# Performance work log

Hardware: AMD Instinct MI355X
Metric: run time of the kernel (lower is better)

Reference implementation:

```python
import jax, jax.numpy as jnp
import numpy as np

N, C, D, H = 4096, 64, 128, 4
CD = 2 * D          # combined_dim = 2*input_size
DQ = CD // 8        # per-head query/key dim


def _mlp(x, W1, b1, W2, b2):
    # MLP(in, hidden, out): Linear -> ReLU -> Linear
    return jax.nn.relu(x @ W1.T + b1) @ W2.T + b2


def _gru(x, h, Wih, bih, Whh, bhh):
    # torch.nn.GRUCell math
    gi = x @ Wih.T + bih
    gh = h @ Whh.T + bhh
    ir, iz, inn = jnp.split(gi, 3, axis=-1)
    hr, hz, hn = jnp.split(gh, 3, axis=-1)
    r = jax.nn.sigmoid(ir + hr)
    z = jax.nn.sigmoid(iz + hz)
    n = jnp.tanh(inn + r * hn)
    return (1.0 - z) * n + z * h


def setup_inputs() -> dict:
    key = jax.random.key(0)
    ks = jax.random.split(key, 16)
    def w(k, shape, fan):
        return jax.random.normal(k, shape, jnp.float32) / np.float32(np.sqrt(fan))
    return {
        "x": jax.random.normal(ks[0], (N, D), jnp.float32),
        "h": jax.random.normal(ks[1], (N, D), jnp.float32),
        "cluster_h": jax.random.normal(ks[2], (C, D), jnp.float32),
        "query_vectors": jax.random.normal(ks[3], (C, D), jnp.float32),
        "cluster_labels": jax.random.randint(ks[4], (N,), 0, C),
        "nodes_ind": jnp.arange(N),
        "edge_index_intra": jax.random.randint(ks[5], (2, 1024), 0, N),
        "num_clusters": C,
        "Wq": w(ks[6], (H, DQ, CD), CD), "bq": jnp.zeros((H, DQ), jnp.float32),
        "Wk": w(ks[7], (H, DQ, CD), CD), "bk": jnp.zeros((H, DQ), jnp.float32),
        "Wv": w(ks[8], (H, CD, CD), CD), "bv": jnp.zeros((H, CD), jnp.float32),
        "W1": w(ks[9], (CD, H * CD), H * CD), "b1": jnp.zeros((CD,), jnp.float32),
        "W2": w(ks[10], (CD, CD), CD), "b2": jnp.zeros((CD,), jnp.float32),
        "gru_Wih": w(ks[11], (3 * D, D), D), "gru_bih": jnp.zeros((3 * D,), jnp.float32),
        "gru_Whh": w(ks[12], (3 * D, D), D), "gru_bhh": jnp.zeros((3 * D,), jnp.float32),
        "Wp": 0.1 * w(ks[13], (D, D), D), "bp": jnp.zeros((D,), jnp.float32),
    }


def reference(x, h, cluster_h, query_vectors, cluster_labels, nodes_ind,
              edge_index_intra, num_clusters,
              Wq, bq, Wk, bk, Wv, bv, W1, b1, W2, b2,
              gru_Wih, gru_bih, gru_Whh, gru_bhh, Wp, bp):
    combined = jnp.concatenate([x, h], axis=-1)              # [N, 2D]
    # multi-head dense attention over all nodes (heads vectorized)
    q = jnp.einsum('nd,hed->hne', combined, Wq) + bq[:, None, :]   # [H,N,DQ]
    k = jnp.einsum('nd,hed->hne', combined, Wk) + bk[:, None, :]
    v = jnp.einsum('nd,hed->hne', combined, Wv) + bv[:, None, :]   # [H,N,2D]
    scores = jnp.einsum('hne,hme->hnm', q, k) / jnp.sqrt(jnp.float32(DQ))
    attn = jax.nn.softmax(jax.nn.leaky_relu(scores, 0.2), axis=-1)  # [H,N,N]
    hp = jnp.einsum('hnm,hme->hne', attn, v)                 # [H,N,2D]
    hp = jnp.transpose(hp, (1, 0, 2)).reshape(combined.shape[0], -1)  # [N,H*2D]
    node_repr = _mlp(hp, W1, b1, W2, b2) + combined          # [N,2D]
    # per-cluster mean of previous node hidden states
    ones = jnp.ones((h.shape[0],), h.dtype)
    counts = jax.ops.segment_sum(ones, cluster_labels, num_segments=num_clusters)
    sums = jax.ops.segment_sum(h, cluster_labels, num_segments=num_clusters)
    agg = sums / jnp.maximum(counts, 1.0)[:, None]           # [C,D]
    present = (counts > 0)[:, None]
    new_ch = _gru(agg, cluster_h, gru_Wih, gru_bih, gru_Whh, gru_bhh)
    updated_cluster_h = jnp.where(present, new_ch, cluster_h)  # [C,D]
    # cluster-to-node projection broadcast back to nodes
    c2n = (updated_cluster_h @ Wp.T + bp)[cluster_labels]    # [N,D]
    updated_h = node_repr[:, D:] + c2n                       # [N,D]
    return updated_h, updated_cluster_h
```

## Files before the change

kernel.cpp:

```cpp
#include <hip/hip_runtime.h>
#include <math.h>

#define N_NODES 4096
#define NHEADS  4
#define NSPLIT  4
#define KVRANGE 1024

typedef _Float16 f16;
typedef _Float16 half8 __attribute__((ext_vector_type(8)));
typedef float f32x4 __attribute__((ext_vector_type(4)));

__global__ __launch_bounds__(256) void k_combined(const float* __restrict__ x,
                                                  const float* __restrict__ h,
                                                  f16* __restrict__ comb16) {
  int i = blockIdx.x * blockDim.x + threadIdx.x;
  int n = i >> 6, c = i & 63;
  float4 v;
  if (c < 32) v = ((const float4*)x)[n * 32 + c];
  else        v = ((const float4*)h)[n * 32 + (c - 32)];
  union { uint2 u; f16 h4[4]; } pk;
  pk.h4[0] = (f16)v.x; pk.h4[1] = (f16)v.y; pk.h4[2] = (f16)v.z; pk.h4[3] = (f16)v.w;
  *(uint2*)&comb16[(size_t)i * 4] = pk.u;
}

__global__ __launch_bounds__(256) void k_w2h(const float* __restrict__ Wq,
                                             const float* __restrict__ Wk,
                                             const float* __restrict__ Wv,
                                             const float* __restrict__ W1,
                                             const float* __restrict__ W2,
                                             f16* __restrict__ pool) {
  int i4 = (blockIdx.x * 256 + threadIdx.x) * 4;
  const float* src; int off;
  if      (i4 <  32768) { src = Wq; off = 0; }
  else if (i4 <  65536) { src = Wk; off = 32768; }
  else if (i4 < 327680) { src = Wv; off = 65536; }
  else if (i4 < 589824) { src = W1; off = 327680; }
  else                  { src = W2; off = 589824; }
  float4 v = *(const float4*)&src[i4 - off];
  union { uint2 u; f16 h4[4]; } pk;
  pk.h4[0] = (f16)v.x; pk.h4[1] = (f16)v.y; pk.h4[2] = (f16)v.z; pk.h4[3] = (f16)v.w;
  *(uint2*)&pool[i4] = pk.u;
}

template <int EPI>
__global__ __launch_bounds__(256) void k_gemm16(const f16* __restrict__ A,
                                                const f16* __restrict__ B,
                                                const float* __restrict__ bias,
                                                const float* __restrict__ resid,
                                                void* __restrict__ outv,
                                                int M, int K, int J, float alpha) {
  __shared__ f16 As[64 * 64];
  __shared__ f16 Bs[64 * 64];
  const int t  = threadIdx.x;
  const int mb = blockIdx.x * 64, jb = blockIdx.y * 64;
  const int w  = t >> 6, l = t & 63;
  const int g_ = l >> 4, c_ = l & 15;
  const int m0 = (w >> 1) * 32, n0 = (w & 1) * 32;

  f32x4 acc[2][2];
#pragma unroll
  for (int i = 0; i < 2; ++i)
#pragma unroll
    for (int j = 0; j < 2; ++j) acc[i][j] = (f32x4){0.f, 0.f, 0.f, 0.f};

#define FRAG16(BUF, row, kh) \
  (*(const half8*)&BUF[(size_t)(row) * 64 + (((((kh) * 4 + g_) ^ (c_ & 7))) << 3)])

  for (int kb = 0; kb < K; kb += 64) {
    __syncthreads();
#pragma unroll
    for (int i = 0; i < 2; ++i) {
      int f = t + i * 256;
      int r = f >> 3, ch = f & 7;
      *(uint4*)&As[r * 64 + ((ch ^ (r & 7)) << 3)] =
          *(const uint4*)&A[(size_t)(mb + r) * K + kb + ch * 8];
      *(uint4*)&Bs[r * 64 + ((ch ^ (r & 7)) << 3)] =
          *(const uint4*)&B[(size_t)(jb + r) * K + kb + ch * 8];
    }
    __syncthreads();
#pragma unroll
    for (int kh = 0; kh < 2; ++kh) {
      half8 a0 = FRAG16(As, m0 + c_, kh);
      half8 a1 = FRAG16(As, m0 + 16 + c_, kh);
      half8 b0 = FRAG16(Bs, n0 + c_, kh);
      half8 b1 = FRAG16(Bs, n0 + 16 + c_, kh);
      acc[0][0] = __builtin_amdgcn_mfma_f32_16x16x32_f16(a0, b0, acc[0][0], 0, 0, 0);
      acc[0][1] = __builtin_amdgcn_mfma_f32_16x16x32_f16(a0, b1, acc[0][1], 0, 0, 0);
      acc[1][0] = __builtin_amdgcn_mfma_f32_16x16x32_f16(a1, b0, acc[1][0], 0, 0, 0);
      acc[1][1] = __builtin_amdgcn_mfma_f32_16x16x32_f16(a1, b1, acc[1][1], 0, 0, 0);
    }
  }
#undef FRAG16

#pragma unroll
  for (int mt = 0; mt < 2; ++mt)
#pragma unroll
    for (int nt = 0; nt < 2; ++nt) {
      int mbase = mb + m0 + mt * 16 + g_ * 4;
      int jj    = jb + n0 + nt * 16 + c_;
      if (EPI == 0 || EPI == 1) {
        f16* out = (f16*)outv;
        float bc = bias[jj];
#pragma unroll
        for (int r = 0; r < 4; ++r) {
          float v = (acc[mt][nt][r] + bc) * alpha;
          if (EPI == 1) v = fmaxf(v, 0.f);
          out[(size_t)(mbase + r) * J + jj] = (f16)v;
        }
      } else if (EPI == 2) {
        f16* out = (f16*)outv;
#pragma unroll
        for (int r = 0; r < 4; ++r)
          out[(size_t)(mbase + r) * J + jj] = (f16)(acc[mt][nt][r] + bias[mbase + r]);
      } else {
        float* out = (float*)outv;
        float bc = bias[jj];
#pragma unroll
        for (int r = 0; r < 4; ++r)
          out[(size_t)(mbase + r) * J + jj] =
              acc[mt][nt][r] + bc + resid[(size_t)(mbase + r) * J + jj];
      }
    }
}

__global__ __launch_bounds__(256, 4) void k_attn_mfma(const f16* __restrict__ qg,
                                                      const f16* __restrict__ kg,
                                                      const f16* __restrict__ vt,
                                                      f16* __restrict__ pO,
                                                      float* __restrict__ pM,
                                                      float* __restrict__ pL) {
  const int hd  = blockIdx.y;
  const int sp  = blockIdx.z;
  const int kv0 = sp * KVRANGE;
  const int t   = threadIdx.x;
  const int w   = t >> 6, l = t & 63;
  const int g   = l >> 4, c = l & 15;
  const int qb  = blockIdx.x * 64 + w * 16;

  __shared__ f16 Ks[32 * 40];
  __shared__ f16 Vs[256 * 40];

  half8 qf = *(const half8*)&qg[(size_t)(qb + c) * 128 + hd * 32 + g * 8];

  f32x4 oacc[16];
#pragma unroll
  for (int i = 0; i < 16; ++i) oacc[i] = (f32x4){0.f, 0.f, 0.f, 0.f};
  float m_run = -INFINITY, l_run = 0.f;

  const int  srcA  = (((2 * g) & 3) << 4) + c;
  const int  srcB  = (((2 * g + 1) & 3) << 4) + c;
  const bool selhi = (g >> 1) != 0;
  const f32x4 zero4 = {0.f, 0.f, 0.f, 0.f};

  for (int kb = 0; kb < KVRANGE; kb += 32) {
    __syncthreads();
    if (t < 128) {
      int r = t >> 2, c8 = (t & 3) * 8;
      *(uint4*)&Ks[r * 40 + c8] =
          *(const uint4*)&kg[(size_t)(kv0 + kb + r) * 128 + hd * 32 + c8];
    }
#pragma unroll
    for (int i = 0; i < 4; ++i) {
      int cc = i * 256 + t, d = cc >> 2, c8 = (cc & 3) * 8;
      *(uint4*)&Vs[d * 40 + c8] =
          *(const uint4*)&vt[(size_t)(hd * 256 + d) * 4096 + kv0 + kb + c8];
    }
    __syncthreads();

    f32x4 s0 = __builtin_amdgcn_mfma_f32_16x16x32_f16(
        *(const half8*)&Ks[(c) * 40 + g * 8], qf, zero4, 0, 0, 0);
    f32x4 s1 = __builtin_amdgcn_mfma_f32_16x16x32_f16(
        *(const half8*)&Ks[(16 + c) * 40 + g * 8], qf, zero4, 0, 0, 0);

    float sv[8];
#pragma unroll
    for (int r = 0; r < 4; ++r) {
      float a = s0[r]; sv[r]     = a > 0.f ? a : 0.2f * a;
      float b = s1[r]; sv[4 + r] = b > 0.f ? b : 0.2f * b;
    }
    float mx = sv[0];
#pragma unroll
    for (int r = 1; r < 8; ++r) mx = fmaxf(mx, sv[r]);
    mx = fmaxf(mx, __shfl_xor(mx, 16));
    mx = fmaxf(mx, __shfl_xor(mx, 32));

    if (!__all(mx <= m_run + 8.f)) {
      float m_new = fmaxf(m_run, mx);
      float cf = __expf(m_run - m_new);
#pragma unroll
      for (int i = 0; i < 16; ++i) {
        oacc[i][0] *= cf; oacc[i][1] *= cf; oacc[i][2] *= cf; oacc[i][3] *= cf;
      }
      l_run *= cf;
      m_run = m_new;
    }
    float p[8], ps = 0.f;
#pragma unroll
    for (int r = 0; r < 8; ++r) { p[r] = __expf(sv[r] - m_run); ps += p[r]; }
    ps += __shfl_xor(ps, 16);
    ps += __shfl_xor(ps, 32);
    l_run += ps;

    unsigned lo0, hi0, lo1, hi1;
    {
      union { unsigned u; f16 h[2]; } z;
      z.h[0] = (f16)p[0]; z.h[1] = (f16)p[1]; lo0 = z.u;
      z.h[0] = (f16)p[2]; z.h[1] = (f16)p[3]; hi0 = z.u;
      z.h[0] = (f16)p[4]; z.h[1] = (f16)p[5]; lo1 = z.u;
      z.h[0] = (f16)p[6]; z.h[1] = (f16)p[7]; hi1 = z.u;
    }
    int A0 = __shfl((int)lo0, srcA), A1 = __shfl((int)hi0, srcA);
    int A2 = __shfl((int)lo1, srcA), A3 = __shfl((int)hi1, srcA);
    int B0 = __shfl((int)lo0, srcB), B1 = __shfl((int)hi0, srcB);
    int B2 = __shfl((int)lo1, srcB), B3 = __shfl((int)hi1, srcB);
    union { half8 v; unsigned u[4]; } pf;
    pf.u[0] = (unsigned)(selhi ? A2 : A0);
    pf.u[1] = (unsigned)(selhi ? A3 : A1);
    pf.u[2] = (unsigned)(selhi ? B2 : B0);
    pf.u[3] = (unsigned)(selhi ? B3 : B1);

#pragma unroll
    for (int dt = 0; dt < 16; ++dt)
      oacc[dt] = __builtin_amdgcn_mfma_f32_16x16x32_f16(
          *(const half8*)&Vs[(dt * 16 + c) * 40 + g * 8], pf.v, oacc[dt], 0, 0, 0);
  }

  float inv = 1.f / l_run;
#pragma unroll
  for (int dt = 0; dt < 16; ++dt) {
#pragma unroll
    for (int r = 0; r < 4; ++r) {
      int j = hd * 256 + dt * 16 + g * 4 + r;
      pO[(size_t)(sp * 1024 + j) * 4096 + qb + c] = (f16)(oacc[dt][r] * inv);
    }
  }
  if (l < 16) {
    pM[(sp * 4 + hd) * 4096 + qb + l] = m_run;
    pL[(sp * 4 + hd) * 4096 + qb + l] = l_run;
  }
}

__global__ __launch_bounds__(256) void k_merge(const f16* __restrict__ pO,
                                               const float* __restrict__ pM,
                                               const float* __restrict__ pL,
                                               f16* __restrict__ hp) {
  const int q0 = blockIdx.x * 64, jb = blockIdx.y * 64;
  const int h  = jb >> 8;
  const int t  = threadIdx.x;
  __shared__ float wm[NSPLIT][64], wl[NSPLIT][64];
  __shared__ float tile[64][65];

  if (t < 64) {
#pragma unroll
    for (int s = 0; s < NSPLIT; ++s) {
      wm[s][t] = pM[(s * 4 + h) * 4096 + q0 + t];
      wl[s][t] = pL[(s * 4 + h) * 4096 + q0 + t];
    }
  }
  __syncthreads();

  const int q8 = (t & 7) * 8;
#pragma unroll
  for (int it = 0; it < 2; ++it) {
    int jl = (t >> 3) + it * 32;
    float wgt[NSPLIT][8], inv[8];
#pragma unroll
    for (int q = 0; q < 8; ++q) {
      float M = wm[0][q8 + q];
#pragma unroll
      for (int s = 1; s < NSPLIT; ++s) M = fmaxf(M, wm[s][q8 + q]);
      float den = 0.f;
#pragma unroll
      for (int s = 0; s < NSPLIT; ++s) {
        float wv = wl[s][q8 + q] * __expf(wm[s][q8 + q] - M);
        wgt[s][q] = wv; den += wv;
      }
      inv[q] = 1.f / den;
    }
    float o[8] = {0.f};
#pragma unroll
    for (int s = 0; s < NSPLIT; ++s) {
      union { uint4 u; f16 h8[8]; } raw;
      raw.u = *(const uint4*)&pO[(size_t)(s * 1024 + jb + jl) * 4096 + q0 + q8];
#pragma unroll
      for (int q = 0; q < 8; ++q) o[q] += wgt[s][q] * (float)raw.h8[q];
    }
#pragma unroll
    for (int q = 0; q < 8; ++q) tile[q8 + q][jl] = o[q] * inv[q];
  }
  __syncthreads();

#pragma unroll
  for (int it = 0; it < 2; ++it) {
    int ql = (t >> 3) + it * 32, chk = t & 7;
    union { uint4 u; f16 h8[8]; } pk;
#pragma unroll
    for (int k = 0; k < 8; ++k) pk.h8[k] = (f16)tile[ql][chk * 8 + k];
    *(uint4*)&hp[(size_t)(q0 + ql) * 1024 + jb + chk * 8] = pk.u;
  }
}

__global__ void k_zero(float* __restrict__ p, int n) {
  int i = blockIdx.x * blockDim.x + threadIdx.x;
  if (i < n) p[i] = 0.f;
}

__global__ __launch_bounds__(256) void k_segsum(const float* __restrict__ h,
                                                const int* __restrict__ lab,
                                                float* __restrict__ sums,
                                                float* __restrict__ cnt) {
  int i = blockIdx.x * blockDim.x + threadIdx.x;
  int n = i >> 7, d = i & 127;
  int c = lab[n];
  atomicAdd(&sums[c * 128 + d], h[i]);
  if (d == 0) atomicAdd(&cnt[c], 1.0f);
}

__global__ __launch_bounds__(128) void k_gru(const float* __restrict__ sums,
                                             const float* __restrict__ cnt,
                                             const float* __restrict__ ch,
                                             const float* __restrict__ Wih,
                                             const float* __restrict__ bih,
                                             const float* __restrict__ Whh,
                                             const float* __restrict__ bhh,
                                             float* __restrict__ uch,
                                             float* __restrict__ out_uch) {
  int c = blockIdx.x, d = threadIdx.x;
  __shared__ float ax[128], hx[128];
  float count = cnt[c];
  ax[d] = sums[c * 128 + d] / fmaxf(count, 1.0f);
  hx[d] = ch[c * 128 + d];
  __syncthreads();
  float gi[3], gh[3];
#pragma unroll
  for (int g = 0; g < 3; ++g) {
    const float* wi = &Wih[(size_t)(g * 128 + d) * 128];
    const float* wh = &Whh[(size_t)(g * 128 + d) * 128];
    float si = 0.f, sh = 0.f;
#pragma unroll 4
    for (int e = 0; e < 128; ++e) {
      si = fmaf(ax[e], wi[e], si);
      sh = fmaf(hx[e], wh[e], sh);
    }
    gi[g] = si + bih[g * 128 + d];
    gh[g] = sh + bhh[g * 128 + d];
  }
  float r = 1.f / (1.f + expf(-(gi[0] + gh[0])));
  float z = 1.f / (1.f + expf(-(gi[1] + gh[1])));
  float nn = tanhf(gi[2] + r * gh[2]);
  float hv = hx[d];
  float nh = (1.f - z) * nn + z * hv;
  float res = (count > 0.f) ? nh : hv;
  uch[c * 128 + d] = res;
  out_uch[c * 128 + d] = res;
}

__global__ __launch_bounds__(128) void k_c2n(const float* __restrict__ uch,
                                             const float* __restrict__ Wp,
                                             const float* __restrict__ bp,
                                             float* __restrict__ c2n) {
  int c = blockIdx.x, d = threadIdx.x;
  __shared__ float u[128];
  u[d] = uch[c * 128 + d];
  __syncthreads();
  const float* w = &Wp[(size_t)d * 128];
  float s = 0.f;
#pragma unroll 4
  for (int e = 0; e < 128; ++e) s = fmaf(u[e], w[e], s);
  c2n[c * 128 + d] = s + bp[d];
}

__global__ __launch_bounds__(256) void k_final(const float* __restrict__ nrh,
                                               const float* __restrict__ c2n,
                                               const int* __restrict__ lab,
                                               float* __restrict__ out) {
  int i = blockIdx.x * blockDim.x + threadIdx.x;
  int n = i >> 7, d = i & 127;
  out[i] = nrh[(size_t)n * 128 + d] + c2n[lab[n] * 128 + d];
}

extern "C" void kernel_launch(void* const* d_in, const int* in_sizes, int n_in,
                              void* d_out, int out_size, void* d_ws, size_t ws_size,
                              hipStream_t stream) {
  const float* x    = (const float*)d_in[0];
  const float* h    = (const float*)d_in[1];
  const float* ch   = (const float*)d_in[2];
  const int*   lab  = (const int*)d_in[4];
  const float* Wq   = (const float*)d_in[8];
  const float* bq   = (const float*)d_in[9];
  const float* Wk   = (const float*)d_in[10];
  const float* bk   = (const float*)d_in[11];
  const float* Wv   = (const float*)d_in[12];
  const float* bv   = (const float*)d_in[13];
  const float* W1   = (const float*)d_in[14];
  const float* b1   = (const float*)d_in[15];
  const float* W2   = (const float*)d_in[16];
  const float* b2   = (const float*)d_in[17];
  const float* gWih = (const float*)d_in[18];
  const float* gbih = (const float*)d_in[19];
  const float* gWhh = (const float*)d_in[20];
  const float* gbhh = (const float*)d_in[21];
  const float* Wp   = (const float*)d_in[22];
  const float* bp   = (const float*)d_in[23];

  float* outp    = (float*)d_out;
  float* out_uch = outp + 4096 * 128;

  f16* comb16 = (f16*)d_ws;
  f16* w16    = comb16 + 4096 * 256;
  f16* wq16   = w16;
  f16* wk16   = w16 + 32768;
  f16* wv16   = w16 + 65536;
  f16* w116   = w16 + 327680;
  f16* w216   = w16 + 589824;
  f16* qf16   = w16 + 655360;
  f16* kf16   = qf16 + 4096 * 128;
  f16* vt16   = kf16 + 4096 * 128;
  f16* pO     = vt16 + 1024 * 4096;
  f16* hp16   = pO + (size_t)NSPLIT * 1024 * 4096;
  f16* y116   = hp16 + (size_t)4096 * 1024;
  float* pM   = (float*)(y116 + 4096 * 256);
  float* pL   = pM + NSPLIT * 4 * 4096;
  float* nrh  = pL + NSPLIT * 4 * 4096;
  float* sums = nrh + 4096 * 128;
  float* cnt  = sums + 64 * 128;
  float* uch  = cnt + 64;
  float* c2n  = uch + 64 * 128;

  const float qscale = 0.17677669529663687f;

  k_combined<<<1024, 256, 0, stream>>>(x, h, comb16);
  k_w2h<<<640, 256, 0, stream>>>(Wq, Wk, Wv, W1, W2, w16);
  k_gemm16<0><<<dim3(64, 2),  256, 0, stream>>>(comb16, wq16, bq, nullptr, qf16, 4096, 256, 128,  qscale);
  k_gemm16<0><<<dim3(64, 2),  256, 0, stream>>>(comb16, wk16, bk, nullptr, kf16, 4096, 256, 128,  1.0f);
  k_gemm16<2><<<dim3(16, 64), 256, 0, stream>>>(wv16, comb16, bv, nullptr, vt16, 1024, 256, 4096, 1.0f);
  k_attn_mfma<<<dim3(64, NHEADS, NSPLIT), 256, 0, stream>>>(qf16, kf16, vt16, pO, pM, pL);
  k_merge<<<dim3(64, 16), 256, 0, stream>>>(pO, pM, pL, hp16);
  k_gemm16<1><<<dim3(64, 4), 256, 0, stream>>>(hp16, w116, b1, nullptr, y116, 4096, 1024, 256, 1.0f);
  k_gemm16<3><<<dim3(64, 2), 256, 0, stream>>>(y116, w216 + 128 * 256, b2 + 128, h, nrh, 4096, 256, 128, 1.0f);
  k_zero<<<33, 256, 0, stream>>>(sums, 64 * 128 + 64);
  k_segsum<<<2048, 256, 0, stream>>>(h, lab, sums, cnt);
  k_gru<<<64, 128, 0, stream>>>(sums, cnt, ch, gWih, gbih, gWhh, gbhh, uch, out_uch);
  k_c2n<<<64, 128, 0, stream>>>(uch, Wp, bp, c2n);
  k_final<<<2048, 256, 0, stream>>>(nrh, c2n, lab, outp);
}
```

Baseline: 287.7 us.

## Share P tiles via LDS in attention, fuse final add into GEMM epilogue

The attention kernel now writes each wave's softmax probabilities and rescale factors to LDS. Each wave then computes a 64-wide slice of the value dimension for all 64 queries, so each V fragment read from LDS is reused across four query tiles instead of being re-read by every wave. This adds a block-wide barrier per KV step and lowers the occupancy hint from 4 to 3. Separately, the cluster-to-node broadcast add is fused into the last GEMM epilogue, which removes the k_final kernel and the nrh buffer, and the GRU and c2n dot loops are vectorized with float4 loads.

After: 270.8 us. -5.9%, faster.

```diff
diff --git a/kernel.cpp b/kernel.cpp
--- a/kernel.cpp
+++ b/kernel.cpp
@@ -47,6 +47,8 @@
                                                 const f16* __restrict__ B,
                                                 const float* __restrict__ bias,
                                                 const float* __restrict__ resid,
+                                                const int* __restrict__ lab,
+                                                const float* __restrict__ c2n,
                                                 void* __restrict__ outv,
                                                 int M, int K, int J, float alpha) {
   __shared__ f16 As[64 * 64];
@@ -116,14 +118,16 @@
         float* out = (float*)outv;
         float bc = bias[jj];
 #pragma unroll
-        for (int r = 0; r < 4; ++r)
-          out[(size_t)(mbase + r) * J + jj] =
-              acc[mt][nt][r] + bc + resid[(size_t)(mbase + r) * J + jj];
+        for (int r = 0; r < 4; ++r) {
+          int m = mbase + r;
+          out[(size_t)m * J + jj] = acc[mt][nt][r] + bc +
+              resid[(size_t)m * J + jj] + c2n[lab[m] * 128 + jj];
+        }
       }
     }
 }
 
-__global__ __launch_bounds__(256, 4) void k_attn_mfma(const f16* __restrict__ qg,
+__global__ __launch_bounds__(256, 3) void k_attn_mfma(const f16* __restrict__ qg,
                                                       const f16* __restrict__ kg,
                                                       const f16* __restrict__ vt,
                                                       f16* __restrict__ pO,
@@ -135,21 +139,21 @@
   const int t   = threadIdx.x;
   const int w   = t >> 6, l = t & 63;
   const int g   = l >> 4, c = l & 15;
-  const int qb  = blockIdx.x * 64 + w * 16;
+  const int qb  = blockIdx.x * 64;
 
   __shared__ f16 Ks[32 * 40];
   __shared__ f16 Vs[256 * 40];
-
-  half8 qf = *(const half8*)&qg[(size_t)(qb + c) * 128 + hd * 32 + g * 8];
-
-  f32x4 oacc[16];
-#pragma unroll
-  for (int i = 0; i < 16; ++i) oacc[i] = (f32x4){0.f, 0.f, 0.f, 0.f};
+  __shared__ f16 Ps[64 * 40];
+  __shared__ float CfS[64];
+
+  half8 qf = *(const half8*)&qg[(size_t)(qb + w * 16 + c) * 128 + hd * 32 + g * 8];
+
+  f32x4 oacc[4][4];
+#pragma unroll
+  for (int i = 0; i < 4; ++i)
+#pragma unroll
+    for (int j = 0; j < 4; ++j) oacc[i][j] = (f32x4){0.f, 0.f, 0.f, 0.f};
   float m_run = -INFINITY, l_run = 0.f;
-
-  const int  srcA  = (((2 * g) & 3) << 4) + c;
-  const int  srcB  = (((2 * g + 1) & 3) << 4) + c;
-  const bool selhi = (g >> 1) != 0;
   const f32x4 zero4 = {0.f, 0.f, 0.f, 0.f};
 
   for (int kb = 0; kb < KVRANGE; kb += 32) {
@@ -184,14 +188,10 @@
     mx = fmaxf(mx, __shfl_xor(mx, 16));
     mx = fmaxf(mx, __shfl_xor(mx, 32));
 
+    float cf = 1.f;
     if (!__all(mx <= m_run + 8.f)) {
       float m_new = fmaxf(m_run, mx);
-      float cf = __expf(m_run - m_new);
-#pragma unroll
-      for (int i = 0; i < 16; ++i) {
-        oacc[i][0] *= cf; oacc[i][1] *= cf; oacc[i][2] *= cf; oacc[i][3] *= cf;
-      }
-      l_run *= cf;
+      cf = __expf(m_run - m_new);
       m_run = m_new;
     }
     float p[8], ps = 0.f;
@@ -199,44 +199,64 @@
     for (int r = 0; r < 8; ++r) { p[r] = __expf(sv[r] - m_run); ps += p[r]; }
     ps += __shfl_xor(ps, 16);
     ps += __shfl_xor(ps, 32);
-    l_run += ps;
-
-    unsigned lo0, hi0, lo1, hi1;
+    l_run = l_run * cf + ps;
+
+    if (g == 0) CfS[w * 16 + c] = cf;
     {
-      union { unsigned u; f16 h[2]; } z;
-      z.h[0] = (f16)p[0]; z.h[1] = (f16)p[1]; lo0 = z.u;
-      z.h[0] = (f16)p[2]; z.h[1] = (f16)p[3]; hi0 = z.u;
-      z.h[0] = (f16)p[4]; z.h[1] = (f16)p[5]; lo1 = z.u;
-      z.h[0] = (f16)p[6]; z.h[1] = (f16)p[7]; hi1 = z.u;
-    }
-    int A0 = __shfl((int)lo0, srcA), A1 = __shfl((int)hi0, srcA);
-    int A2 = __shfl((int)lo1, srcA), A3 = __shfl((int)hi1, srcA);
-    int B0 = __shfl((int)lo0, srcB), B1 = __shfl((int)hi0, srcB);
-    int B2 = __shfl((int)lo1, srcB), B3 = __shfl((int)hi1, srcB);
-    union { half8 v; unsigned u[4]; } pf;
-    pf.u[0] = (unsigned)(selhi ? A2 : A0);
-    pf.u[1] = (unsigned)(selhi ? A3 : A1);
-    pf.u[2] = (unsigned)(selhi ? B2 : B0);
-    pf.u[3] = (unsigned)(selhi ? B3 : B1);
-
-#pragma unroll
-    for (int dt = 0; dt < 16; ++dt)
-      oacc[dt] = __builtin_amdgcn_mfma_f32_16x16x32_f16(
-          *(const half8*)&Vs[(dt * 16 + c) * 40 + g * 8], pf.v, oacc[dt], 0, 0, 0);
-  }
-
-  float inv = 1.f / l_run;
-#pragma unroll
-  for (int dt = 0; dt < 16; ++dt) {
-#pragma unroll
-    for (int r = 0; r < 4; ++r) {
-      int j = hd * 256 + dt * 16 + g * 4 + r;
-      pO[(size_t)(sp * 1024 + j) * 4096 + qb + c] = (f16)(oacc[dt][r] * inv);
-    }
-  }
-  if (l < 16) {
-    pM[(sp * 4 + hd) * 4096 + qb + l] = m_run;
-    pL[(sp * 4 + hd) * 4096 + qb + l] = l_run;
+      union { unsigned u; f16 h2[2]; } z;
+      uint2 lo, hi;
+      z.h2[0] = (f16)p[0]; z.h2[1] = (f16)p[1]; lo.x = z.u;
+      z.h2[0] = (f16)p[2]; z.h2[1] = (f16)p[3]; lo.y = z.u;
+      z.h2[0] = (f16)p[4]; z.h2[1] = (f16)p[5]; hi.x = z.u;
+      z.h2[0] = (f16)p[6]; z.h2[1] = (f16)p[7]; hi.y = z.u;
+      *(uint2*)&Ps[(w * 16 + c) * 40 + g * 4]      = lo;
+      *(uint2*)&Ps[(w * 16 + c) * 40 + 16 + g * 4] = hi;
+    }
+    __syncthreads();
+
+#pragma unroll
+    for (int qt = 0; qt < 4; ++qt) {
+      float cfq = CfS[qt * 16 + c];
+      if (!__all(cfq == 1.f)) {
+#pragma unroll
+        for (int i = 0; i < 4; ++i) {
+          oacc[i][qt][0] *= cfq; oacc[i][qt][1] *= cfq;
+          oacc[i][qt][2] *= cfq; oacc[i][qt][3] *= cfq;
+        }
+      }
+    }
+    half8 pfr[4];
+#pragma unroll
+    for (int qt = 0; qt < 4; ++qt)
+      pfr[qt] = *(const half8*)&Ps[(qt * 16 + c) * 40 + g * 8];
+#pragma unroll
+    for (int i = 0; i < 4; ++i) {
+      half8 vfr = *(const half8*)&Vs[((w * 4 + i) * 16 + c) * 40 + g * 8];
+#pragma unroll
+      for (int qt = 0; qt < 4; ++qt)
+        oacc[i][qt] = __builtin_amdgcn_mfma_f32_16x16x32_f16(vfr, pfr[qt], oacc[i][qt], 0, 0, 0);
+    }
+  }
+
+  __syncthreads();
+  if (g == 0) CfS[w * 16 + c] = l_run;
+  __syncthreads();
+  float linv[4];
+#pragma unroll
+  for (int qt = 0; qt < 4; ++qt) linv[qt] = 1.f / CfS[qt * 16 + c];
+#pragma unroll
+  for (int i = 0; i < 4; ++i)
+#pragma unroll
+    for (int qt = 0; qt < 4; ++qt)
+#pragma unroll
+      for (int r = 0; r < 4; ++r) {
+        int j = hd * 256 + (w * 4 + i) * 16 + g * 4 + r;
+        pO[(size_t)(sp * 1024 + j) * 4096 + qb + qt * 16 + c] =
+            (f16)(oacc[i][qt][r] * linv[qt]);
+      }
+  if (g == 0) {
+    pM[(sp * 4 + hd) * 4096 + qb + w * 16 + c] = m_run;
+    pL[(sp * 4 + hd) * 4096 + qb + w * 16 + c] = l_run;
   }
 }
 
@@ -334,13 +354,16 @@
   float gi[3], gh[3];
 #pragma unroll
   for (int g = 0; g < 3; ++g) {
-    const float* wi = &Wih[(size_t)(g * 128 + d) * 128];
-    const float* wh = &Whh[(size_t)(g * 128 + d) * 128];
+    const float4* wi4 = (const float4*)&Wih[(size_t)(g * 128 + d) * 128];
+    const float4* wh4 = (const float4*)&Whh[(size_t)(g * 128 + d) * 128];
     float si = 0.f, sh = 0.f;
-#pragma unroll 4
-    for (int e = 0; e < 128; ++e) {
-      si = fmaf(ax[e], wi[e], si);
-      sh = fmaf(hx[e], wh[e], sh);
+#pragma unroll 8
+    for (int e = 0; e < 32; ++e) {
+      float4 wv = wi4[e], hv = wh4[e];
+      si = fmaf(ax[e*4+0], wv.x, si); si = fmaf(ax[e*4+1], wv.y, si);
+      si = fmaf(ax[e*4+2], wv.z, si); si = fmaf(ax[e*4+3], wv.w, si);
+      sh = fmaf(hx[e*4+0], hv.x, sh); sh = fmaf(hx[e*4+1], hv.y, sh);
+      sh = fmaf(hx[e*4+2], hv.z, sh); sh = fmaf(hx[e*4+3], hv.w, sh);
     }
     gi[g] = si + bih[g * 128 + d];
     gh[g] = sh + bhh[g * 128 + d];
@@ -363,20 +386,15 @@
   __shared__ float u[128];
   u[d] = uch[c * 128 + d];
   __syncthreads();
-  const float* w = &Wp[(size_t)d * 128];
+  const float4* w4 = (const float4*)&Wp[(size_t)d * 128];
   float s = 0.f;
-#pragma unroll 4
-  for (int e = 0; e < 128; ++e) s = fmaf(u[e], w[e], s);
+#pragma unroll 8
+  for (int e = 0; e < 32; ++e) {
+    float4 wv = w4[e];
+    s = fmaf(u[e*4+0], wv.x, s); s = fmaf(u[e*4+1], wv.y, s);
+    s = fmaf(u[e*4+2], wv.z, s); s = fmaf(u[e*4+3], wv.w, s);
+  }
   c2n[c * 128 + d] = s + bp[d];
-}
-
-__global__ __launch_bounds__(256) void k_final(const float* __restrict__ nrh,
-                                               const float* __restrict__ c2n,
-                                               const int* __restrict__ lab,
-                                               float* __restrict__ out) {
-  int i = blockIdx.x * blockDim.x + threadIdx.x;
-  int n = i >> 7, d = i & 127;
-  out[i] = nrh[(size_t)n * 128 + d] + c2n[lab[n] * 128 + d];
 }
 
 extern "C" void kernel_launch(void* const* d_in, const int* in_sizes, int n_in,
@@ -421,8 +439,7 @@
   f16* y116   = hp16 + (size_t)4096 * 1024;
   float* pM   = (float*)(y116 + 4096 * 256);
   float* pL   = pM + NSPLIT * 4 * 4096;
-  float* nrh  = pL + NSPLIT * 4 * 4096;
-  float* sums = nrh + 4096 * 128;
+  float* sums = pL + NSPLIT * 4 * 4096;
   float* cnt  = sums + 64 * 128;
   float* uch  = cnt + 64;
   float* c2n  = uch + 64 * 128;
@@ -431,16 +448,15 @@
 
   k_combined<<<1024, 256, 0, stream>>>(x, h, comb16);
   k_w2h<<<640, 256, 0, stream>>>(Wq, Wk, Wv, W1, W2, w16);
-  k_gemm16<0><<<dim3(64, 2),  256, 0, stream>>>(comb16, wq16, bq, nullptr, qf16, 4096, 256, 128,  qscale);
-  k_gemm16<0><<<dim3(64, 2),  256, 0, stream>>>(comb16, wk16, bk, nullptr, kf16, 4096, 256, 128,  1.0f);
-  k_gemm16<2><<<dim3(16, 64), 256, 0, stream>>>(wv16, comb16, bv, nullptr, vt16, 1024, 256, 4096, 1.0f);
+  k_gemm16<0><<<dim3(64, 2),  256, 0, stream>>>(comb16, wq16, bq, nullptr, nullptr, nullptr, qf16, 4096, 256, 128,  qscale);
+  k_gemm16<0><<<dim3(64, 2),  256, 0, stream>>>(comb16, wk16, bk, nullptr, nullptr, nullptr, kf16, 4096, 256, 128,  1.0f);
+  k_gemm16<2><<<dim3(16, 64), 256, 0, stream>>>(wv16, comb16, bv, nullptr, nullptr, nullptr, vt16, 1024, 256, 4096, 1.0f);
   k_attn_mfma<<<dim3(64, NHEADS, NSPLIT), 256, 0, stream>>>(qf16, kf16, vt16, pO, pM, pL);
   k_merge<<<dim3(64, 16), 256, 0, stream>>>(pO, pM, pL, hp16);
-  k_gemm16<1><<<dim3(64, 4), 256, 0, stream>>>(hp16, w116, b1, nullptr, y116, 4096, 1024, 256, 1.0f);
-  k_gemm16<3><<<dim3(64, 2), 256, 0, stream>>>(y116, w216 + 128 * 256, b2 + 128, h, nrh, 4096, 256, 128, 1.0f);
+  k_gemm16<1><<<dim3(64, 4), 256, 0, stream>>>(hp16, w116, b1, nullptr, nullptr, nullptr, y116, 4096, 1024, 256, 1.0f);
   k_zero<<<33, 256, 0, stream>>>(sums, 64 * 128 + 64);
   k_segsum<<<2048, 256, 0, stream>>>(h, lab, sums, cnt);
   k_gru<<<64, 128, 0, stream>>>(sums, cnt, ch, gWih, gbih, gWhh, gbhh, uch, out_uch);
   k_c2n<<<64, 128, 0, stream>>>(uch, Wp, bp, c2n);
-  k_final<<<2048, 256, 0, stream>>>(nrh, c2n, lab, outp);
-}
+  k_gemm16<3><<<dim3(64, 2), 256, 0, stream>>>(y116, w216 + 128 * 256, b2 + 128, h, lab, c2n, outp, 4096, 256, 128, 1.0f);
+}
```
